# Kernel tuning notes

Measured on AMD Instinct MI355X. Metric: run time of the kernel, lower is better.

Reference implementation:

```python
import jax, jax.numpy as jnp
from jax import lax
import numpy as np

T, B, IN, H = 192, 16, 256, 256


def setup_inputs() -> dict:
    key = jax.random.key(0)
    ks = jax.random.split(key, 8)
    s = 0.05  # small init scale to keep gates well-conditioned
    return {
        "x": jax.random.normal(ks[0], (T, B, IN), dtype=jnp.float32),
        # shared LSTM (PyTorch gate order i,f,g,o)
        "W_ih": jax.random.normal(ks[1], (4 * H, IN), dtype=jnp.float32) * s,
        "W_hh": jax.random.normal(ks[2], (4 * H, H), dtype=jnp.float32) * s,
        "b_lstm": jnp.zeros((4 * H,), dtype=jnp.float32),
        # additive attention: Ws: (IN+2H)->H, Us: H->1
        "Ws_w": jax.random.normal(ks[3], (H, IN + 2 * H), dtype=jnp.float32) * s,
        "Ws_b": jnp.zeros((H,), dtype=jnp.float32),
        "Us_w": jax.random.normal(ks[4], (1, H), dtype=jnp.float32) * s,
        "Us_b": jnp.zeros((1,), dtype=jnp.float32),
        # task-specific message LSTM cell: gates from concat(x_t, Rt, h_prev)
        "Wc": jax.random.normal(ks[5], (4 * H, IN + 2 * H), dtype=jnp.float32) * s,
        "bc": jnp.zeros((4 * H,), dtype=jnp.float32),
        "TASK": 0,
    }


def _lstm_gates(pre, c):
    i, f, g, o = jnp.split(pre, 4, axis=-1)
    i = jax.nn.sigmoid(i)
    f = jax.nn.sigmoid(f)
    g = jnp.tanh(g)
    o = jax.nn.sigmoid(o)
    c_new = f * c + i * g
    h_new = o * jnp.tanh(c_new)
    return h_new, c_new


def reference(x, W_ih, W_hh, b_lstm, Ws_w, Ws_b, Us_w, Us_b, Wc, bc, TASK):
    t_len, b, _ = x.shape
    h = W_hh.shape[1]

    h0 = jnp.zeros((b, h), x.dtype)

    # ---- shared LSTM over time ----
    def shared_step(carry, xt):
        hh, cc = carry
        pre = xt @ W_ih.T + hh @ W_hh.T + b_lstm
        hh, cc = _lstm_gates(pre, cc)
        return (hh, cc), hh

    (_, _), hs = lax.scan(shared_step, (h0, h0), x)  # hs: [T,B,H]

    # ---- per-timestep additive attention + message LSTM cell ----
    def task_step(carry, xt):
        hh, cc = carry
        h_task = jnp.broadcast_to(hh[None], (t_len, b, h))
        cat = jnp.concatenate([hs, h_task, x], axis=-1)          # [T,B,IN+2H]
        score = jnp.tanh(cat @ Ws_w.T + Ws_b) @ Us_w.T + Us_b    # [T,B,1]
        att = jax.nn.softmax(score, axis=0)                       # over time
        Rt = jnp.sum(att * hs, axis=0)                            # [B,H]
        pre = jnp.concatenate([xt, Rt, hh], axis=-1) @ Wc.T + bc
        hh, cc = _lstm_gates(pre, cc)
        return (hh, cc), hh

    (_, _), outs = lax.scan(task_step, (h0, h0), x)  # [T,B,H]
    return jnp.transpose(outs, (1, 0, 2))  # [B,T,H] (torch.stack axis=1)
```

## Files before the change

kernel.cpp:

```cpp
#include <hip/hip_runtime.h>
#include <hip/hip_fp16.h>

#define T_LEN 192

typedef unsigned long long u64;
typedef _Float16 f16x8 __attribute__((ext_vector_type(8)));
typedef float f32x4 __attribute__((ext_vector_type(4)));

#define OFF_X1F   0
#define OFF_XPRE  3145728
#define OFF_XB3   6291456
#define OFF_HSB   7077888
#define OFF_P     7864320
#define OFF_R     7913472
#define OFF_H     7921664
#define OFF_HX    7929856
#define EXCH_WORDS 81920

#define SMEM_TASK 148736

__device__ __forceinline__ unsigned packh2(float a, float b){
  union { __half2 h; unsigned u; } v;
  v.h = __halves2half2(__float2half(a), __float2half(b));
  return v.u;
}
__device__ __forceinline__ float2 unp2(unsigned u){
  union { unsigned u32; __half2 h; } v; v.u32 = u;
  return __half22float2(v.h);
}
__device__ __forceinline__ float fdot2(unsigned a, unsigned b, float c){
#if __has_builtin(__builtin_amdgcn_fdot2)
  typedef _Float16 h2t __attribute__((ext_vector_type(2)));
  union { unsigned u; h2t h; } ua, ub;
  ua.u = a; ub.u = b;
  return __builtin_amdgcn_fdot2(ua.h, ub.h, c, false);
#else
  float2 x = unp2(a), y = unp2(b);
  return c + x.x*y.x + x.y*y.y;
#endif
}
__device__ __forceinline__ float tanh_f(float x){
  float cx = fminf(fmaxf(x, -15.f), 15.f);
  float e = __expf(2.f * cx);
  return (e - 1.f) / (e + 1.f);
}
__device__ __forceinline__ float sigm(float x){
  float cx = fminf(fmaxf(x, -30.f), 30.f);
  return 1.f / (1.f + __expf(-cx));
}

__device__ __forceinline__ u64 gld64(const u64* p){
  return __hip_atomic_load(p, __ATOMIC_RELAXED, __HIP_MEMORY_SCOPE_AGENT);
}
__device__ __forceinline__ void gst64(u64* p, u64 v){
  __hip_atomic_store(p, v, __ATOMIC_RELAXED, __HIP_MEMORY_SCOPE_AGENT);
}

__global__ __launch_bounds__(256) void initk(float* p, int n){
  int i = blockIdx.x * blockDim.x + threadIdx.x;
  int stride = gridDim.x * blockDim.x;
  for (; i < n; i += stride) p[i] = 0.f;
}

__global__ __launch_bounds__(256) void proj3(const float* __restrict__ x,
                                             const float* __restrict__ W_ih,
                                             const float* __restrict__ b_l,
                                             const float* __restrict__ Wc,
                                             const float* __restrict__ bc,
                                             const float* __restrict__ Ws_w,
                                             const float* __restrict__ Ws_b,
                                             float* __restrict__ ws){
  __shared__ float As[16 * 258];
  __shared__ float Wsh[256 * 34];
  const int bx = blockIdx.x, t = blockIdx.y, tid = threadIdx.x;
  const float* W; const float* bias; int ldw, woff, c0, mode; float* out;
  if (bx < 32)      { W = W_ih; bias = b_l;  ldw = 256; woff = 0;   c0 = bx * 32;        mode = 0; out = ws + OFF_X1F; }
  else if (bx < 64) { W = Wc;   bias = bc;   ldw = 768; woff = 0;   c0 = (bx - 32) * 32; mode = 1; out = ws + OFF_XPRE; }
  else              { W = Ws_w; bias = Ws_b; ldw = 768; woff = 512; c0 = (bx - 64) * 32; mode = 2; out = ws + OFF_XB3; }

  for (int i = 0; i < 16; ++i)
    As[i * 258 + tid] = x[(t * 16 + i) * 256 + tid];
  for (int i = 0; i < 32; ++i)
    Wsh[tid * 34 + i] = W[(c0 + i) * ldw + woff + tid];
  __syncthreads();

  const int r = tid >> 4;
  const int c2 = (tid & 15) * 2;
  float acc0 = 0.f, acc1 = 0.f;
  for (int k = 0; k < 256; k += 2) {
    float2 a  = *(const float2*)&As[r * 258 + k];
    float2 w0 = *(const float2*)&Wsh[k * 34 + c2];
    float2 w1 = *(const float2*)&Wsh[(k + 1) * 34 + c2];
    acc0 = fmaf(a.x, w0.x, acc0); acc0 = fmaf(a.y, w1.x, acc0);
    acc1 = fmaf(a.x, w0.y, acc1); acc1 = fmaf(a.y, w1.y, acc1);
  }
  const int cg = c0 + c2;
  acc0 += bias[cg]; acc1 += bias[cg + 1];
  float2 res; res.x = acc0; res.y = acc1;
  if (mode == 0) {
    *(float2*)&out[((t * 64 + (cg >> 4)) * 16 + r) * 16 + (cg & 15)] = res;
  } else if (mode == 1) {
    *(float2*)&out[(t * 16 + r) * 1024 + cg] = res;
  } else {
    *(float2*)&out[(t * 16 + r) * 256 + cg] = res;
  }
}

__global__ __launch_bounds__(512) void lstm_kernel(const float* __restrict__ X1F,
                                                   const float* __restrict__ W_hh,
                                                   float* __restrict__ hsB,
                                                   u64* __restrict__ hx){
  __shared__ unsigned hT[16 * 136];
  const int tid = threadIdx.x;
  const int wg = blockIdx.x;
  const int wave = tid >> 6, lane = tid & 63;
  const int b16 = lane & 15, quad = lane >> 4;
  const int jb = wg * 8 + wave;
  const int peer0 = (1 - wg) * 128;

  f16x8 wf[4][8];
  #pragma unroll
  for (int g = 0; g < 4; ++g) {
    #pragma unroll
    for (int kk = 0; kk < 8; ++kk) {
      int row = g * 256 + jb * 16 + b16;
      const float* wp = &W_hh[row * 256 + kk * 32 + quad * 8];
      f16x8 v;
      #pragma unroll
      for (int j = 0; j < 8; ++j) v[j] = (_Float16)wp[j];
      wf[g][kk] = v;
    }
  }
  for (int i = tid; i < 16 * 136; i += 512) hT[i] = 0u;
  float cst[4] = {0.f, 0.f, 0.f, 0.f};
  __syncthreads();

  for (int t = 0; t < T_LEN; ++t) {
    float4 xi[4];
    #pragma unroll
    for (int g = 0; g < 4; ++g)
      xi[g] = *(const float4*)&X1F[((t * 64 + g * 16 + jb) * 16 + b16) * 16 + quad * 4];

    if (t > 0) {
      const u64* src = &hx[((u64)((t - 1) & 1) * 256) * 16];
      #pragma unroll
      for (int cc = 0; cc < 2; ++cc) {
        int idx = tid * 2 + cc;
        int jp = idx >> 4, bbq = idx & 15;
        int j0 = peer0 + jp * 2;
        u64 v0, v1;
        for (;;) {
          v0 = gld64(&src[(j0) * 16 + bbq]);
          v1 = gld64(&src[(j0 + 1) * 16 + bbq]);
          if ((unsigned)v0 == (unsigned)t && (unsigned)v1 == (unsigned)t) break;
        }
        hT[bbq * 136 + (j0 >> 1)] =
            packh2(__uint_as_float((unsigned)(v0 >> 32)),
                   __uint_as_float((unsigned)(v1 >> 32)));
      }
    }
    __syncthreads();

    f32x4 acc[4];
    #pragma unroll
    for (int g = 0; g < 4; ++g) {
      f32x4 a; a[0]=xi[g].x; a[1]=xi[g].y; a[2]=xi[g].z; a[3]=xi[g].w;
      acc[g] = a;
    }
    #pragma unroll
    for (int kk = 0; kk < 8; ++kk) {
      union { uint4 u; f16x8 h; } bv;
      bv.u = *(const uint4*)&hT[b16 * 136 + kk * 16 + quad * 4];
      #pragma unroll
      for (int g = 0; g < 4; ++g)
        acc[g] = __builtin_amdgcn_mfma_f32_16x16x32_f16(wf[g][kk], bv.h, acc[g], 0, 0, 0);
    }
    __syncthreads();

    float hv[4];
    #pragma unroll
    for (int r = 0; r < 4; ++r) {
      float pi = acc[0][r], pf = acc[1][r], pg = acc[2][r], po = acc[3][r];
      float cn = fmaf(sigm(pf), cst[r], sigm(pi) * tanh_f(pg));
      hv[r] = sigm(po) * tanh_f(cn);
      cst[r] = cn;
    }
    int j0 = jb * 16 + quad * 4;
    *(float4*)&hsB[(b16 * 192 + t) * 256 + j0] = make_float4(hv[0], hv[1], hv[2], hv[3]);
    hT[b16 * 136 + (j0 >> 1)]     = packh2(hv[0], hv[1]);
    hT[b16 * 136 + (j0 >> 1) + 1] = packh2(hv[2], hv[3]);
    u64* dst = &hx[((u64)(t & 1) * 256) * 16];
    #pragma unroll
    for (int r = 0; r < 4; ++r)
      gst64(&dst[(j0 + r) * 16 + b16],
            ((u64)__float_as_uint(hv[r]) << 32) | (unsigned)(t + 1));
  }
}

__global__ __launch_bounds__(1024) void task_kernel(
    const float* __restrict__ xb3, const float* __restrict__ xpre,
    const float* __restrict__ hsB, const float* __restrict__ Us_w,
    const float* __restrict__ Us_b, const float* __restrict__ Wc,
    const float* __restrict__ Ws_w,
    u64* __restrict__ Pbuf, u64* __restrict__ Hbuf,
    float* __restrict__ out){
  extern __shared__ char smem[];
  unsigned* hsL  = (unsigned*)smem;
  unsigned* Ws1L = (unsigned*)(smem + 99072);
  float*    baseS= (float*)(smem + 115584);
  unsigned* WcH  = (unsigned*)smem;
  unsigned* Ws2L = (unsigned*)(smem + 65536);
  float* scr     = (float*)(smem + 82176);
  float* prel    = (float*)(smem + 82176);
  float* eel     = (float*)(smem + 86400);
  unsigned* h2l  = (unsigned*)(smem + 87168);
  unsigned* actH = (unsigned*)(smem + 87680);
  float* hterml  = (float*)(smem + 88192);
  float* usl     = (float*)(smem + 88320);
  float* msc     = (float*)(smem + 88448);
  unsigned* G2   = (unsigned*)(smem + 99072);

  const int tid = threadIdx.x;
  const int bb = blockIdx.x & 15;
  const int s  = blockIdx.x >> 4;

  for (int idx = tid; idx < 24576; idx += 1024) {
    int tp = idx >> 7, k2 = idx & 127;
    const float* hp = &hsB[(bb * 192 + tp) * 256 + 2 * k2];
    hsL[tp * 129 + k2] = packh2(hp[0], hp[1]);
  }
  for (int idx = tid; idx < 4096; idx += 1024) {
    int c = idx >> 7, k2 = idx & 127;
    const float* wp = &Ws_w[(32 * s + c) * 768 + 2 * k2];
    Ws1L[c * 129 + k2] = packh2(wp[0], wp[1]);
  }
  __syncthreads();
  {
    int c = tid & 31, g = tid >> 5;
    float a6[6];
    #pragma unroll
    for (int j = 0; j < 6; ++j)
      a6[j] = xb3[((g * 6 + j) * 16 + bb) * 256 + 32 * s + c];
    for (int k2 = 0; k2 < 128; ++k2) {
      unsigned wv = Ws1L[c * 129 + k2];
      #pragma unroll
      for (int j = 0; j < 6; ++j)
        a6[j] = fdot2(wv, hsL[(g * 6 + j) * 129 + k2], a6[j]);
    }
    #pragma unroll
    for (int j = 0; j < 6; ++j)
      baseS[(g * 6 + j) * 33 + c] = a6[j];
  }
  __syncthreads();
  unsigned bs4[4] = {0u, 0u, 0u, 0u};
  if (tid < 768) {
    int tp = tid >> 2, q = tid & 3;
    #pragma unroll
    for (int j2 = 0; j2 < 4; ++j2)
      bs4[j2] = packh2(baseS[tp * 33 + q * 8 + 2 * j2],
                       baseS[tp * 33 + q * 8 + 2 * j2 + 1]);
  }
  __syncthreads();
  {
    int l = tid & 127, tg = tid >> 7;
    int row = (l >> 5) * 256 + 32 * s + (l & 31);
    const float* wr = &Wc[row * 768 + 256];
    float acc[24];
    #pragma unroll
    for (int i = 0; i < 24; ++i) acc[i] = 0.f;
    for (int kc = 0; kc < 128; kc += 16) {
      unsigned wv[16];
      #pragma unroll
      for (int i = 0; i < 16; ++i) {
        float2 wp2 = *(const float2*)&wr[2 * (kc + i)];
        wv[i] = packh2(wp2.x, wp2.y);
      }
      #pragma unroll
      for (int tt = 0; tt < 24; ++tt) {
        const unsigned* hp = &hsL[(tg * 24 + tt) * 129 + kc];
        float a = acc[tt];
        #pragma unroll
        for (int i = 0; i < 16; ++i) a = fdot2(wv[i], hp[i], a);
        acc[tt] = a;
      }
    }
    #pragma unroll
    for (int i = 0; i < 12; ++i)
      G2[l * 97 + tg * 12 + i] = packh2(acc[2 * i], acc[2 * i + 1]);
  }
  __syncthreads();
  for (int idx = tid; idx < 16384; idx += 1024) {
    int j = idx & 3, l = (idx >> 2) & 127, k2q = idx >> 9;
    int k2 = k2q * 4 + j;
    int row = (l >> 5) * 256 + 32 * s + (l & 31);
    const float* wp = &Wc[row * 768 + 512 + 2 * k2];
    WcH[idx] = packh2(wp[0], wp[1]);
  }
  for (int idx = tid; idx < 4096; idx += 1024) {
    int c = idx >> 7, k2 = idx & 127;
    const float* wp = &Ws_w[(32 * s + c) * 768 + 256 + 2 * k2];
    Ws2L[c * 130 + k2] = packh2(wp[0], wp[1]);
  }
  if (tid < 32) usl[tid] = Us_w[32 * s + tid];
  const float usb = Us_b[0];
  __syncthreads();

  u64* Pb = Pbuf + (bb * 8) * 192;
  u64* Hb = Hbuf + bb * 256;
  const uint4* wp4 = (const uint4*)WcH;
  const uint4* av4 = (const uint4*)actH;
  float creg = 0.f;

  for (int t = 0; t < T_LEN; ++t) {
    const unsigned seq = (unsigned)(t + 1);
    float xp0 = 0.f, xp1 = 0.f, xp2 = 0.f, xp3 = 0.f;
    if (tid < 32) {
      const float* xq = &xpre[(t * 16 + bb) * 1024 + 32 * s + tid];
      xp0 = xq[0]; xp1 = xq[256]; xp2 = xq[512]; xp3 = xq[768];
    }
    if (tid < 256) {
      float hvv = 0.f;
      if (t > 0) {
        u64 v;
        do { v = gld64(&Hb[tid]); } while ((unsigned)v != (unsigned)t);
        hvv = __uint_as_float((unsigned)(v >> 32));
      }
      float hp_ = __shfl_xor(hvv, 1);
      if ((tid & 1) == 0) {
        unsigned u = packh2(hvv, hp_);
        h2l[tid >> 1] = u; actH[tid >> 1] = u;
      }
    }
    __syncthreads();
    {
      int c = tid & 31, seg = tid >> 5;
      float a = 0.f;
      #pragma unroll
      for (int i = 0; i < 4; ++i)
        a = fdot2(Ws2L[c * 130 + seg * 4 + i], h2l[seg * 4 + i], a);
      scr[c * 33 + seg] = a;
    }
    __syncthreads();
    if (tid < 32) {
      float a = 0.f;
      #pragma unroll 8
      for (int i = 0; i < 32; ++i) a += scr[tid * 33 + i];
      hterml[tid] = a;
    }
    __syncthreads();
    if (tid < 768) {
      int tp = tid >> 2, q = tid & 3;
      float p = 0.f;
      #pragma unroll
      for (int m = 0; m < 4; ++m) {
        float2 bv = unp2(bs4[m]);
        int c0 = q * 8 + 2 * m;
        p += usl[c0]     * tanh_f(bv.x + hterml[c0]);
        p += usl[c0 + 1] * tanh_f(bv.y + hterml[c0 + 1]);
      }
      p += __shfl_xor(p, 1);
      p += __shfl_xor(p, 2);
      if ((tid & 3) == 0)
        gst64(&Pb[s * 192 + tp], ((u64)__float_as_uint(p) << 32) | seq);
    }
    if (tid < 192) {
      u64 v[8];
      for (;;) {
        bool ok = true;
        #pragma unroll
        for (int sp = 0; sp < 8; ++sp) {
          v[sp] = gld64(&Pb[sp * 192 + tid]);
          ok &= ((unsigned)v[sp] == seq);
        }
        if (ok) break;
      }
      float sum = 0.f;
      #pragma unroll
      for (int sp = 0; sp < 8; ++sp) sum += __uint_as_float((unsigned)(v[sp] >> 32));
      eel[tid] = __expf(sum + usb);
    }
    __syncthreads();
    if (tid < 64) {
      float aa = eel[tid] + eel[tid + 64] + eel[tid + 128];
      #pragma unroll
      for (int off = 32; off >= 1; off >>= 1) aa += __shfl_xor(aa, off);
      if (tid == 0) msc[0] = 1.f / aa;
    }
    {
      int l = tid & 127, kq = tid >> 7;
      float a = 0.f;
      if (kq < 4) {
        #pragma unroll
        for (int i = 0; i < 8; ++i) {
          uint4 w4 = wp4[(kq * 8 + i) * 128 + l];
          uint4 a4 = av4[kq * 8 + i];
          a = fdot2(w4.x, a4.x, a); a = fdot2(w4.y, a4.y, a);
          a = fdot2(w4.z, a4.z, a); a = fdot2(w4.w, a4.w, a);
        }
      } else {
        int l4 = kq - 4;
        const unsigned* gp = &G2[l * 97 + l4 * 24];
        const float2* ep = (const float2*)&eel[l4 * 48];
        #pragma unroll
        for (int i = 0; i < 24; ++i) {
          float2 g = unp2(gp[i]);
          float2 e = ep[i];
          a = fmaf(g.x, e.x, a); a = fmaf(g.y, e.y, a);
        }
      }
      prel[l * 8 + kq] = a;
    }
    __syncthreads();
    if (tid < 32) {
      float m = msc[0];
      float pr[4];
      #pragma unroll
      for (int g = 0; g < 4; ++g) {
        const float4* pp = (const float4*)&prel[(g * 32 + tid) * 8];
        float4 p0 = pp[0], p1 = pp[1];
        pr[g] = (p0.x + p0.y + p0.z + p0.w) + m * (p1.x + p1.y + p1.z + p1.w);
      }
      pr[0] += xp0; pr[1] += xp1; pr[2] += xp2; pr[3] += xp3;
      float cn = fmaf(sigm(pr[1]), creg, sigm(pr[0]) * tanh_f(pr[2]));
      float hh = sigm(pr[3]) * tanh_f(cn);
      creg = cn;
      out[(bb * 192 + t) * 256 + 32 * s + tid] = hh;
      gst64(&Hb[32 * s + tid], ((u64)__float_as_uint(hh) << 32) | seq);
    }
  }
}

extern "C" void kernel_launch(void* const* d_in, const int* in_sizes, int n_in,
                              void* d_out, int out_size, void* d_ws, size_t ws_size,
                              hipStream_t stream) {
  (void)in_sizes; (void)n_in; (void)out_size; (void)ws_size;
  const float* x    = (const float*)d_in[0];
  const float* W_ih = (const float*)d_in[1];
  const float* W_hh = (const float*)d_in[2];
  const float* b_l  = (const float*)d_in[3];
  const float* Ws_w = (const float*)d_in[4];
  const float* Ws_b = (const float*)d_in[5];
  const float* Us_w = (const float*)d_in[6];
  const float* Us_b = (const float*)d_in[7];
  const float* Wc   = (const float*)d_in[8];
  const float* bc   = (const float*)d_in[9];
  float* out = (float*)d_out;
  float* ws = (float*)d_ws;

  hipFuncSetAttribute((const void*)task_kernel,
                      hipFuncAttributeMaxDynamicSharedMemorySize, 160 * 1024);

  initk<<<64, 256, 0, stream>>>(ws + OFF_P, EXCH_WORDS);

  proj3<<<dim3(72, 192), 256, 0, stream>>>(x, W_ih, b_l, Wc, bc, Ws_w, Ws_b, ws);

  lstm_kernel<<<2, 512, 0, stream>>>(ws + OFF_X1F, W_hh, ws + OFF_HSB,
                                     (u64*)(ws + OFF_HX));

  task_kernel<<<128, 1024, SMEM_TASK, stream>>>(
      ws + OFF_XB3, ws + OFF_XPRE, ws + OFF_HSB, Us_w, Us_b, Wc, Ws_w,
      (u64*)(ws + OFF_P), (u64*)(ws + OFF_H), out);
}
```

Before: 1.789 ms.

## Exchange partial attention projections across blocks and pack LSTM h exchange as fp16 pairs

In the task kernel, each block now computes the Ws_h·h contribution for its own 32 hidden units against all 256 output columns and publishes it through a new global exchange buffer. Blocks then gather the partial sums with a shuffle reduction instead of each recomputing a full 256x32 product after a barrier. The Wc·h matvec is split so it can start while waiting on attention scores. In the shared LSTM kernel, hidden states are exchanged as packed fp16 pairs, halving the polling loads. This adds another global exchange round and an extra barrier per step.

```diff
diff --git a/kernel.cpp b/kernel.cpp
--- a/kernel.cpp
+++ b/kernel.cpp
@@ -12,10 +12,10 @@
 #define OFF_XB3   6291456
 #define OFF_HSB   7077888
 #define OFF_P     7864320
-#define OFF_R     7913472
 #define OFF_H     7921664
 #define OFF_HX    7929856
-#define EXCH_WORDS 81920
+#define OFF_HP    7946240
+#define EXCH_WORDS 147456
 
 #define SMEM_TASK 148736
 
@@ -116,7 +116,7 @@
   const int wave = tid >> 6, lane = tid & 63;
   const int b16 = lane & 15, quad = lane >> 4;
   const int jb = wg * 8 + wave;
-  const int peer0 = (1 - wg) * 128;
+  const int jpbase = (1 - wg) * 64;
 
   f16x8 wf[4][8];
   #pragma unroll
@@ -142,21 +142,15 @@
       xi[g] = *(const float4*)&X1F[((t * 64 + g * 16 + jb) * 16 + b16) * 16 + quad * 4];
 
     if (t > 0) {
-      const u64* src = &hx[((u64)((t - 1) & 1) * 256) * 16];
+      const u64* src = &hx[((u64)((t - 1) & 1) * 128) * 16];
       #pragma unroll
       for (int cc = 0; cc < 2; ++cc) {
         int idx = tid * 2 + cc;
-        int jp = idx >> 4, bbq = idx & 15;
-        int j0 = peer0 + jp * 2;
-        u64 v0, v1;
-        for (;;) {
-          v0 = gld64(&src[(j0) * 16 + bbq]);
-          v1 = gld64(&src[(j0 + 1) * 16 + bbq]);
-          if ((unsigned)v0 == (unsigned)t && (unsigned)v1 == (unsigned)t) break;
-        }
-        hT[bbq * 136 + (j0 >> 1)] =
-            packh2(__uint_as_float((unsigned)(v0 >> 32)),
-                   __uint_as_float((unsigned)(v1 >> 32)));
+        int jpp = idx >> 4, bbq = idx & 15;
+        int jp = jpbase + jpp;
+        u64 v;
+        do { v = gld64(&src[jp * 16 + bbq]); } while ((unsigned)v != (unsigned)t);
+        hT[bbq * 136 + jp] = (unsigned)(v >> 32);
       }
     }
     __syncthreads();
@@ -186,14 +180,15 @@
       cst[r] = cn;
     }
     int j0 = jb * 16 + quad * 4;
+    int jp = j0 >> 1;
+    unsigned p01 = packh2(hv[0], hv[1]);
+    unsigned p23 = packh2(hv[2], hv[3]);
+    u64* dst = &hx[((u64)(t & 1) * 128) * 16];
+    gst64(&dst[(jp)     * 16 + b16], ((u64)p01 << 32) | (unsigned)(t + 1));
+    gst64(&dst[(jp + 1) * 16 + b16], ((u64)p23 << 32) | (unsigned)(t + 1));
     *(float4*)&hsB[(b16 * 192 + t) * 256 + j0] = make_float4(hv[0], hv[1], hv[2], hv[3]);
-    hT[b16 * 136 + (j0 >> 1)]     = packh2(hv[0], hv[1]);
-    hT[b16 * 136 + (j0 >> 1) + 1] = packh2(hv[2], hv[3]);
-    u64* dst = &hx[((u64)(t & 1) * 256) * 16];
-    #pragma unroll
-    for (int r = 0; r < 4; ++r)
-      gst64(&dst[(j0 + r) * 16 + b16],
-            ((u64)__float_as_uint(hv[r]) << 32) | (unsigned)(t + 1));
+    hT[b16 * 136 + jp]     = p01;
+    hT[b16 * 136 + jp + 1] = p23;
   }
 }
 
@@ -202,22 +197,21 @@
     const float* __restrict__ hsB, const float* __restrict__ Us_w,
     const float* __restrict__ Us_b, const float* __restrict__ Wc,
     const float* __restrict__ Ws_w,
-    u64* __restrict__ Pbuf, u64* __restrict__ Hbuf,
+    u64* __restrict__ Pbuf, u64* __restrict__ Hbuf, u64* __restrict__ HPbuf,
     float* __restrict__ out){
   extern __shared__ char smem[];
   unsigned* hsL  = (unsigned*)smem;
   unsigned* Ws1L = (unsigned*)(smem + 99072);
   float*    baseS= (float*)(smem + 115584);
   unsigned* WcH  = (unsigned*)smem;
-  unsigned* Ws2L = (unsigned*)(smem + 65536);
-  float* scr     = (float*)(smem + 82176);
-  float* prel    = (float*)(smem + 82176);
-  float* eel     = (float*)(smem + 86400);
-  unsigned* h2l  = (unsigned*)(smem + 87168);
-  unsigned* actH = (unsigned*)(smem + 87680);
-  float* hterml  = (float*)(smem + 88192);
-  float* usl     = (float*)(smem + 88320);
-  float* msc     = (float*)(smem + 88448);
+  unsigned* Ws2P = (unsigned*)(smem + 65536);
+  float* prel    = (float*)(smem + 82944);
+  float* eel     = (float*)(smem + 89600);
+  unsigned* h2l  = (unsigned*)(smem + 90368);
+  unsigned* h2own= (unsigned*)(smem + 90880);
+  float* hterml  = (float*)(smem + 90944);
+  float* usl     = (float*)(smem + 91072);
+  float* msc     = (float*)(smem + 91200);
   unsigned* G2   = (unsigned*)(smem + 99072);
 
   const int tid = threadIdx.x;
@@ -297,18 +291,19 @@
     WcH[idx] = packh2(wp[0], wp[1]);
   }
   for (int idx = tid; idx < 4096; idx += 1024) {
-    int c = idx >> 7, k2 = idx & 127;
-    const float* wp = &Ws_w[(32 * s + c) * 768 + 256 + 2 * k2];
-    Ws2L[c * 130 + k2] = packh2(wp[0], wp[1]);
+    int c = idx >> 4, j = idx & 15;
+    const float* wp = &Ws_w[c * 768 + 256 + 2 * (16 * s + j)];
+    Ws2P[c * 17 + j] = packh2(wp[0], wp[1]);
   }
   if (tid < 32) usl[tid] = Us_w[32 * s + tid];
   const float usb = Us_b[0];
   __syncthreads();
 
-  u64* Pb = Pbuf + (bb * 8) * 192;
-  u64* Hb = Hbuf + bb * 256;
+  u64* Pb  = Pbuf + (bb * 8) * 192;
+  u64* Hb  = Hbuf + bb * 256;
+  u64* HPb = HPbuf + (bb * 8) * 256;
   const uint4* wp4 = (const uint4*)WcH;
-  const uint4* av4 = (const uint4*)actH;
+  const uint4* av4 = (const uint4*)h2l;
   float creg = 0.f;
 
   for (int t = 0; t < T_LEN; ++t) {
@@ -318,34 +313,25 @@
       const float* xq = &xpre[(t * 16 + bb) * 1024 + 32 * s + tid];
       xp0 = xq[0]; xp1 = xq[256]; xp2 = xq[512]; xp3 = xq[768];
     }
-    if (tid < 256) {
-      float hvv = 0.f;
-      if (t > 0) {
+    if (t > 0) {
+      if (tid < 256) {
+        int c = tid >> 3, sp = tid & 7;
         u64 v;
-        do { v = gld64(&Hb[tid]); } while ((unsigned)v != (unsigned)t);
-        hvv = __uint_as_float((unsigned)(v >> 32));
-      }
-      float hp_ = __shfl_xor(hvv, 1);
-      if ((tid & 1) == 0) {
-        unsigned u = packh2(hvv, hp_);
-        h2l[tid >> 1] = u; actH[tid >> 1] = u;
-      }
-    }
-    __syncthreads();
-    {
-      int c = tid & 31, seg = tid >> 5;
-      float a = 0.f;
-      #pragma unroll
-      for (int i = 0; i < 4; ++i)
-        a = fdot2(Ws2L[c * 130 + seg * 4 + i], h2l[seg * 4 + i], a);
-      scr[c * 33 + seg] = a;
-    }
-    __syncthreads();
-    if (tid < 32) {
-      float a = 0.f;
-      #pragma unroll 8
-      for (int i = 0; i < 32; ++i) a += scr[tid * 33 + i];
-      hterml[tid] = a;
+        do { v = gld64(&HPb[sp * 256 + 32 * s + c]); } while ((unsigned)v != (unsigned)t);
+        float a = __uint_as_float((unsigned)(v >> 32));
+        a += __shfl_xor(a, 1); a += __shfl_xor(a, 2); a += __shfl_xor(a, 4);
+        if (sp == 0) hterml[c] = a;
+      } else if (tid < 512) {
+        int col = tid - 256;
+        u64 v;
+        do { v = gld64(&Hb[col]); } while ((unsigned)v != (unsigned)t);
+        float hvv = __uint_as_float((unsigned)(v >> 32));
+        float hp_ = __shfl_xor(hvv, 1);
+        if ((col & 1) == 0) h2l[col >> 1] = packh2(hvv, hp_);
+      }
+    } else {
+      if (tid < 32) hterml[tid] = 0.f;
+      if (tid < 128) h2l[tid] = 0u;
     }
     __syncthreads();
     if (tid < 768) {
@@ -362,6 +348,18 @@
       p += __shfl_xor(p, 2);
       if ((tid & 3) == 0)
         gst64(&Pb[s * 192 + tp], ((u64)__float_as_uint(p) << 32) | seq);
+    }
+    {
+      int l = tid & 127, kq = tid >> 7;
+      float a = 0.f;
+      #pragma unroll
+      for (int i = 0; i < 4; ++i) {
+        uint4 w4 = wp4[(kq * 4 + i) * 128 + l];
+        uint4 a4 = av4[kq * 4 + i];
+        a = fdot2(w4.x, a4.x, a); a = fdot2(w4.y, a4.y, a);
+        a = fdot2(w4.z, a4.z, a); a = fdot2(w4.w, a4.w, a);
+      }
+      prel[l * 13 + kq] = a;
     }
     if (tid < 192) {
       u64 v[8];
@@ -386,29 +384,18 @@
       for (int off = 32; off >= 1; off >>= 1) aa += __shfl_xor(aa, off);
       if (tid == 0) msc[0] = 1.f / aa;
     }
-    {
-      int l = tid & 127, kq = tid >> 7;
+    if (tid >= 512) {
+      int l = (tid - 512) & 127, tq = (tid - 512) >> 7;
+      const unsigned* gp = &G2[l * 97 + tq * 24];
+      const float2* ep = (const float2*)&eel[tq * 48];
       float a = 0.f;
-      if (kq < 4) {
-        #pragma unroll
-        for (int i = 0; i < 8; ++i) {
-          uint4 w4 = wp4[(kq * 8 + i) * 128 + l];
-          uint4 a4 = av4[kq * 8 + i];
-          a = fdot2(w4.x, a4.x, a); a = fdot2(w4.y, a4.y, a);
-          a = fdot2(w4.z, a4.z, a); a = fdot2(w4.w, a4.w, a);
-        }
-      } else {
-        int l4 = kq - 4;
-        const unsigned* gp = &G2[l * 97 + l4 * 24];
-        const float2* ep = (const float2*)&eel[l4 * 48];
-        #pragma unroll
-        for (int i = 0; i < 24; ++i) {
-          float2 g = unp2(gp[i]);
-          float2 e = ep[i];
-          a = fmaf(g.x, e.x, a); a = fmaf(g.y, e.y, a);
-        }
-      }
-      prel[l * 8 + kq] = a;
+      #pragma unroll
+      for (int i = 0; i < 24; ++i) {
+        float2 g = unp2(gp[i]);
+        float2 e = ep[i];
+        a = fmaf(g.x, e.x, a); a = fmaf(g.y, e.y, a);
+      }
+      prel[l * 13 + 8 + tq] = a;
     }
     __syncthreads();
     if (tid < 32) {
@@ -416,16 +403,27 @@
       float pr[4];
       #pragma unroll
       for (int g = 0; g < 4; ++g) {
-        const float4* pp = (const float4*)&prel[(g * 32 + tid) * 8];
-        float4 p0 = pp[0], p1 = pp[1];
-        pr[g] = (p0.x + p0.y + p0.z + p0.w) + m * (p1.x + p1.y + p1.z + p1.w);
+        const float* pp = &prel[(g * 32 + tid) * 13];
+        float hsum = pp[0] + pp[1] + pp[2] + pp[3] + pp[4] + pp[5] + pp[6] + pp[7];
+        float gsum = pp[8] + pp[9] + pp[10] + pp[11];
+        pr[g] = hsum + m * gsum;
       }
       pr[0] += xp0; pr[1] += xp1; pr[2] += xp2; pr[3] += xp3;
       float cn = fmaf(sigm(pr[1]), creg, sigm(pr[0]) * tanh_f(pr[2]));
       float hh = sigm(pr[3]) * tanh_f(cn);
       creg = cn;
+      gst64(&Hb[32 * s + tid], ((u64)__float_as_uint(hh) << 32) | seq);
       out[(bb * 192 + t) * 256 + 32 * s + tid] = hh;
-      gst64(&Hb[32 * s + tid], ((u64)__float_as_uint(hh) << 32) | seq);
+      float hp_ = __shfl_xor(hh, 1);
+      if ((tid & 1) == 0) h2own[tid >> 1] = packh2(hh, hp_);
+    }
+    __syncthreads();
+    if (tid < 256) {
+      float a = 0.f;
+      const unsigned* wp = &Ws2P[tid * 17];
+      #pragma unroll
+      for (int j = 0; j < 16; ++j) a = fdot2(wp[j], h2own[j], a);
+      gst64(&HPb[s * 256 + tid], ((u64)__float_as_uint(a) << 32) | seq);
     }
   }
 }
@@ -459,5 +457,5 @@
 
   task_kernel<<<128, 1024, SMEM_TASK, stream>>>(
       ws + OFF_XB3, ws + OFF_XPRE, ws + OFF_HSB, Us_w, Us_b, Wc, Ws_w,
-      (u64*)(ws + OFF_P), (u64*)(ws + OFF_H), out);
-}
+      (u64*)(ws + OFF_P), (u64*)(ws + OFF_H), (u64*)(ws + OFF_HP), out);
+}
```

Result: faster. 1.713 ms (-4.3%).
